# Optimization experiments

Hardware: AMD Instinct MI355X
Metric: run time of the kernel (lower is better)

## Reference

```python
import jax, jax.numpy as jnp
import numpy as np

EPS = 1e-08


def setup_inputs() -> dict:
    key = jax.random.key(0)
    ks = jax.random.split(key, 9)
    B, T, H, W = 128, 32, 32, 32
    Z = 128
    d = {}
    d['x_seq'] = jax.random.normal(ks[0], (B, T, H, W), dtype=jnp.float32)
    # encoder MLP: 1024 -> 256 -> 128 (kaiming-ish scale)
    d['We1'] = jax.random.normal(ks[1], (H * W, 256), dtype=jnp.float32) * (2.0 / (H * W)) ** 0.5
    d['be1'] = jnp.zeros((256,), jnp.float32)
    d['We2'] = jax.random.normal(ks[2], (256, Z), dtype=jnp.float32) * (2.0 / 256) ** 0.5
    d['be2'] = jnp.zeros((Z,), jnp.float32)
    # context norm params
    d['gamma'] = jnp.ones((Z,), jnp.float32)
    d['beta'] = jnp.zeros((Z,), jnp.float32)
    # g_theta: (128+1)*2=258 -> 512 -> 256
    d['Wg1'] = jax.random.normal(ks[3], (258, 512), dtype=jnp.float32) * (2.0 / 258) ** 0.5
    d['bg1'] = jnp.zeros((512,), jnp.float32)
    d['Wg2'] = jax.random.normal(ks[4], (512, 256), dtype=jnp.float32) * (2.0 / 512) ** 0.5
    d['bg2'] = jnp.zeros((256,), jnp.float32)
    # f_phi: 256 -> 256 -> y_dim=4
    d['Wf'] = jax.random.normal(ks[5], (256, 256), dtype=jnp.float32) * (2.0 / 256) ** 0.5
    d['bf'] = jnp.zeros((256,), jnp.float32)
    d['Wy'] = jax.random.normal(ks[6], (256, 4), dtype=jnp.float32) * (1.0 / 256) ** 0.5
    d['by'] = jnp.zeros((4,), jnp.float32)
    return d


def reference(x_seq, We1, be1, We2, be2, gamma, beta, Wg1, bg1, Wg2, bg2, Wf, bf, Wy, by):
    B, T, H, W = x_seq.shape
    # Encoder (MLP stand-in), vectorized over the sequence dim
    x = x_seq.reshape(B, T, H * W)
    h = jax.nn.relu(jnp.einsum('btd,dk->btk', x, We1) + be1)
    z = jnp.einsum('btk,kz->btz', h, We2) + be2          # [B,T,128]
    # Context norm over the sequence dim (torch .var() is unbiased, ddof=1)
    mu = z.mean(axis=1, keepdims=True)
    sigma = jnp.sqrt(z.var(axis=1, keepdims=True, ddof=1) + EPS)
    z = (z - mu) / sigma * gamma + beta
    # Append temporal tag
    tag = jnp.broadcast_to(jnp.arange(T, dtype=z.dtype)[None, :, None], (B, T, 1))
    z = jnp.concatenate([z, tag], axis=2)                # [B,T,129]
    # Relation network over all T^2 ordered pairs, batched as one GEMM.
    # g_hidden = relu([z_i, z_j] @ Wg1 + bg1); split Wg1 to avoid materializing the concat.
    Wg1_a, Wg1_b = Wg1[:129], Wg1[129:]
    gi = jnp.einsum('bic,ch->bih', z, Wg1_a)             # [B,T,512]
    gj = jnp.einsum('bjc,ch->bjh', z, Wg1_b)             # [B,T,512]
    g_hidden = jax.nn.relu(gi[:, :, None, :] + gj[:, None, :, :] + bg1)  # [B,T,T,512]
    g_out = jax.nn.relu(jnp.einsum('bijh,hg->bijg', g_hidden, Wg2) + bg2)
    all_g = g_out.sum(axis=(1, 2))                       # [B,256]
    f_hidden = jax.nn.relu(all_g @ Wf + bf)
    y_pred_linear = f_hidden @ Wy + by                   # [B,4]
    y_pred = jnp.argmax(y_pred_linear, axis=1)
    return (y_pred_linear, y_pred)
```

## Files before the change

### kernel.cpp

```cpp
#include <hip/hip_runtime.h>
#include <hip/hip_bf16.h>

#define EPS 1e-8f

typedef __attribute__((ext_vector_type(8))) short short8;
typedef __attribute__((ext_vector_type(4))) float f32x4;
typedef __attribute__((ext_vector_type(16))) float f32x16;

__device__ __forceinline__ unsigned short f2bf(float f) {
  union { float f; unsigned u; } v; v.f = f;
  unsigned r = v.u + 0x7fffu + ((v.u >> 16) & 1u);
  return (unsigned short)(r >> 16);
}
__device__ __forceinline__ float bf2f(unsigned short b) {
  union { unsigned u; float f; } v; v.u = ((unsigned)b) << 16;
  return v.f;
}
__device__ __forceinline__ unsigned pack_bf2(float lo, float hi) {
  unsigned r;
  asm("v_cvt_pk_bf16_f32 %0, %1, %2" : "=v"(r) : "v"(lo), "v"(hi));
  return r;
}

__global__ __launch_bounds__(256) void k0_prep(const float* __restrict__ We1,
                                               const float* __restrict__ We2,
                                               const float* __restrict__ Wg1,
                                               const float* __restrict__ Wg2,
                                               const float* __restrict__ Wf,
                                               unsigned short* __restrict__ We1T,
                                               unsigned short* __restrict__ We2T,
                                               unsigned short* __restrict__ Wg1T,
                                               unsigned short* __restrict__ Wg2T,
                                               unsigned short* __restrict__ WfT) {
  int idx = blockIdx.x * 256 + threadIdx.x;
  if (idx < 262144) {
    int n = idx >> 10, k = idx & 1023;
    We1T[idx] = f2bf(We1[k * 256 + n]);
  } else if (idx < 294912) {
    int e = idx - 262144;
    int n = e >> 8, k = e & 255;
    We2T[e] = f2bf(We2[k * 128 + n]);
  } else if (idx < 458752) {
    int e = idx - 294912;
    int n = e / 160, c = e % 160;
    float v = 0.f;
    if (c < 129) v = (n < 512) ? Wg1[c * 512 + n] : Wg1[(129 + c) * 512 + (n - 512)];
    Wg1T[e] = f2bf(v);
  } else if (idx < 589824) {
    int e = idx - 458752;
    int n = e >> 9, k = e & 511;
    Wg2T[e] = f2bf(Wg2[k * 256 + n]);
  } else {
    int e = idx - 589824;
    int n = e >> 8, k = e & 255;
    WfT[e] = f2bf(Wf[k * 256 + n]);
  }
}

__global__ __launch_bounds__(512, 2) void k1(const float* __restrict__ x,
                                             const unsigned short* __restrict__ We1T,
                                             const float* __restrict__ be1,
                                             unsigned short* __restrict__ h_bf) {
  __shared__ unsigned char As[2][8192];
  int tid = threadIdx.x, lane = tid & 63, w = tid >> 6;
  int m0 = blockIdx.x * 16;
  int srow = tid >> 5, skk = (tid & 31) * 8;
  int cb = w * 32;
  int row = lane & 15, kg = (lane >> 4) * 8;

  f32x4 acc[2] = {{0,0,0,0},{0,0,0,0}};

  auto stage = [&](int kc, int buf) {
    const float* src = x + (size_t)(m0 + srow) * 1024 + kc * 256 + skk;
    float4 a = *reinterpret_cast<const float4*>(src);
    float4 b = *reinterpret_cast<const float4*>(src + 4);
    uint4 pv;
    pv.x = pack_bf2(a.x, a.y); pv.y = pack_bf2(a.z, a.w);
    pv.z = pack_bf2(b.x, b.y); pv.w = pack_bf2(b.z, b.w);
    int addr = (srow * 512 + skk * 2) ^ ((srow & 7) << 4);
    *reinterpret_cast<uint4*>(&As[buf][addr]) = pv;
  };

  stage(0, 0);
  __syncthreads();
  for (int kc = 0; kc < 4; ++kc) {
    if (kc < 3) stage(kc + 1, (kc + 1) & 1);
    short8 breg[2][8];
#pragma unroll
    for (int cf = 0; cf < 2; ++cf)
#pragma unroll
      for (int ks = 0; ks < 8; ++ks)
        breg[cf][ks] = *reinterpret_cast<const short8*>(
            We1T + (size_t)(cb + cf * 16 + row) * 1024 + kc * 256 + ks * 32 + kg);
    const unsigned char* hc = &As[kc & 1][0];
#pragma unroll
    for (int ks = 0; ks < 8; ++ks) {
      int aoff = (row * 512 + ks * 64 + kg * 2) ^ ((row & 7) << 4);
      short8 af = *reinterpret_cast<const short8*>(hc + aoff);
      acc[0] = __builtin_amdgcn_mfma_f32_16x16x32_bf16(af, breg[0][ks], acc[0], 0, 0, 0);
      acc[1] = __builtin_amdgcn_mfma_f32_16x16x32_bf16(af, breg[1][ks], acc[1], 0, 0, 0);
    }
    __syncthreads();
  }
#pragma unroll
  for (int cf = 0; cf < 2; ++cf) {
    int col = cb + cf * 16 + row;
    float bias = be1[col];
#pragma unroll
    for (int r = 0; r < 4; ++r) {
      int orow = m0 + (lane >> 4) * 4 + r;
      h_bf[(size_t)orow * 256 + col] = f2bf(fmaxf(acc[cf][r] + bias, 0.f));
    }
  }
}

__global__ __launch_bounds__(256) void k2(const unsigned short* __restrict__ h_bf,
                                          const unsigned short* __restrict__ We2T,
                                          const float* __restrict__ be2,
                                          const float* __restrict__ gamma,
                                          const float* __restrict__ beta,
                                          const unsigned short* __restrict__ Wg1T,
                                          const float* __restrict__ bg1,
                                          unsigned short* __restrict__ g_all) {
  __shared__ unsigned char zcs[16384];
  __shared__ float zb[32][132];
  int b = blockIdx.x >> 2, nq = blockIdx.x & 3;
  int tid = threadIdx.x, lane = tid & 63, w = tid >> 6;
  int row = lane & 15, kg = (lane >> 4) * 8;

  {
    int srow = tid >> 3, skk = (tid & 7) * 32;
#pragma unroll
    for (int q = 0; q < 4; ++q) {
      short8 v = *reinterpret_cast<const short8*>(
          h_bf + (size_t)(b * 32 + srow) * 256 + skk + q * 8);
      int addr = (srow * 512 + (skk + q * 8) * 2) ^ ((srow & 7) << 4);
      *reinterpret_cast<short8*>(&zcs[addr]) = v;
    }
  }
  short8 breg1[2][8];
#pragma unroll
  for (int cf = 0; cf < 2; ++cf)
#pragma unroll
    for (int ks = 0; ks < 8; ++ks)
      breg1[cf][ks] = *reinterpret_cast<const short8*>(
          We2T + (size_t)(w * 32 + cf * 16 + row) * 256 + ks * 32 + kg);
  __syncthreads();

  {
    f32x4 acc[2][2] = {{{0,0,0,0},{0,0,0,0}},{{0,0,0,0},{0,0,0,0}}};
#pragma unroll
    for (int ks = 0; ks < 8; ++ks) {
      int a0off = (row * 512 + ks * 64 + kg * 2) ^ ((row & 7) << 4);
      int a1off = ((16 + row) * 512 + ks * 64 + kg * 2) ^ ((row & 7) << 4);
      short8 a0 = *reinterpret_cast<const short8*>(&zcs[a0off]);
      short8 a1 = *reinterpret_cast<const short8*>(&zcs[a1off]);
#pragma unroll
      for (int cf = 0; cf < 2; ++cf) {
        acc[0][cf] = __builtin_amdgcn_mfma_f32_16x16x32_bf16(a0, breg1[cf][ks], acc[0][cf], 0, 0, 0);
        acc[1][cf] = __builtin_amdgcn_mfma_f32_16x16x32_bf16(a1, breg1[cf][ks], acc[1][cf], 0, 0, 0);
      }
    }
#pragma unroll
    for (int rf = 0; rf < 2; ++rf)
#pragma unroll
      for (int cf = 0; cf < 2; ++cf) {
        int col = w * 32 + cf * 16 + row;
        float bias = be2[col];
#pragma unroll
        for (int r = 0; r < 4; ++r)
          zb[rf * 16 + (lane >> 4) * 4 + r][col] = acc[rf][cf][r] + bias;
      }
  }
  __syncthreads();

  if (tid < 128) {
    float s = 0.f, s2 = 0.f;
#pragma unroll 4
    for (int t = 0; t < 32; ++t) { float v = zb[t][tid]; s += v; s2 += v * v; }
    float mu = s * (1.f / 32.f);
    float var = (s2 - 32.f * mu * mu) * (1.f / 31.f);
    float rs = 1.f / sqrtf(fmaxf(var, 0.f) + EPS);
    float g = gamma[tid], be = beta[tid];
#pragma unroll 4
    for (int t = 0; t < 32; ++t) {
      unsigned short v = f2bf((zb[t][tid] - mu) * rs * g + be);
      int addr = (t * 512 + tid * 2) ^ ((t & 7) << 4);
      *reinterpret_cast<unsigned short*>(&zcs[addr]) = v;
    }
  } else if (tid < 160) {
    for (int t = 0; t < 32; ++t) {
      unsigned short v = (tid == 128) ? f2bf((float)t) : 0;
      int addr = (t * 512 + tid * 2) ^ ((t & 7) << 4);
      *reinterpret_cast<unsigned short*>(&zcs[addr]) = v;
    }
  }
  __syncthreads();

  {
    int n0 = nq * 256 + w * 64;
    short8 af[2][5];
#pragma unroll
    for (int rf = 0; rf < 2; ++rf)
#pragma unroll
      for (int ks = 0; ks < 5; ++ks) {
        int aoff = ((rf * 16 + row) * 512 + ks * 64 + kg * 2) ^ ((row & 7) << 4);
        af[rf][ks] = *reinterpret_cast<const short8*>(&zcs[aoff]);
      }
    short8 breg[4][5];
#pragma unroll
    for (int cf = 0; cf < 4; ++cf)
#pragma unroll
      for (int ks = 0; ks < 5; ++ks)
        breg[cf][ks] = *reinterpret_cast<const short8*>(
            Wg1T + (size_t)(n0 + cf * 16 + row) * 160 + ks * 32 + kg);
    f32x4 acc[2][4] = {{{0,0,0,0},{0,0,0,0},{0,0,0,0},{0,0,0,0}},
                       {{0,0,0,0},{0,0,0,0},{0,0,0,0},{0,0,0,0}}};
#pragma unroll
    for (int ks = 0; ks < 5; ++ks)
#pragma unroll
      for (int cf = 0; cf < 4; ++cf) {
        acc[0][cf] = __builtin_amdgcn_mfma_f32_16x16x32_bf16(af[0][ks], breg[cf][ks], acc[0][cf], 0, 0, 0);
        acc[1][cf] = __builtin_amdgcn_mfma_f32_16x16x32_bf16(af[1][ks], breg[cf][ks], acc[1][cf], 0, 0, 0);
      }
#pragma unroll
    for (int cf = 0; cf < 4; ++cf) {
      int n = n0 + cf * 16 + row;
      float bias = (n < 512) ? bg1[n] : 0.f;
#pragma unroll
      for (int rf = 0; rf < 2; ++rf)
#pragma unroll
        for (int r = 0; r < 4; ++r) {
          int t = rf * 16 + (lane >> 4) * 4 + r;
          g_all[((size_t)(b * 32 + t) << 10) + n] = f2bf(acc[rf][cf][r] + bias);
        }
    }
  }
}

__global__ __launch_bounds__(512, 2) void k3(const unsigned short* __restrict__ g_all,
                                             const unsigned short* __restrict__ Wg2T,
                                             const float* __restrict__ bg2,
                                             float* __restrict__ all_gp) {
  __shared__ unsigned char ldsH[2][32768];
  int b = blockIdx.x >> 1, hi = blockIdx.x & 1;
  int ii0 = hi * 16;
  int tid = threadIdx.x, lane = tid & 63, w = tid >> 6;
  int l31 = lane & 31, lhi = lane >> 5;
  int cb = w * 32;
  int p = tid >> 4, kslot = tid & 15;

  short8 breg[32];
#pragma unroll
  for (int s = 0; s < 32; ++s)
    breg[s] = *reinterpret_cast<const short8*>(
        Wg2T + (size_t)(cb + l31) * 512 + s * 16 + lhi * 8);

  float gjf[32];
  {
    const unsigned short* gjp = g_all + ((size_t)(b * 32 + p) << 10) + 512 + kslot * 8;
#pragma unroll
    for (int q = 0; q < 4; ++q) {
      short8 gv0 = *reinterpret_cast<const short8*>(gjp + q * 128);
#pragma unroll
      for (int e = 0; e < 8; ++e) gjf[q * 8 + e] = bf2f((unsigned short)gv0[e]);
    }
  }
  float bias = bg2[cb + l31];
  float accsum = 0.f;

  short8 gv[4];
  auto hload = [&](int ii) {
    const unsigned short* gi = g_all + ((size_t)(b * 32 + ii) << 10) + kslot * 8;
#pragma unroll
    for (int q = 0; q < 4; ++q)
      gv[q] = *reinterpret_cast<const short8*>(gi + q * 128);
  };
  auto hstore = [&](int buf) {
    unsigned char* hb = &ldsH[buf][0] + p * 1024;
#pragma unroll
    for (int q = 0; q < 4; ++q) {
      uint4 pv;
      float f0 = fmaxf(bf2f((unsigned short)gv[q][0]) + gjf[q * 8 + 0], 0.f);
      float f1 = fmaxf(bf2f((unsigned short)gv[q][1]) + gjf[q * 8 + 1], 0.f);
      float f2 = fmaxf(bf2f((unsigned short)gv[q][2]) + gjf[q * 8 + 2], 0.f);
      float f3 = fmaxf(bf2f((unsigned short)gv[q][3]) + gjf[q * 8 + 3], 0.f);
      float f4 = fmaxf(bf2f((unsigned short)gv[q][4]) + gjf[q * 8 + 4], 0.f);
      float f5 = fmaxf(bf2f((unsigned short)gv[q][5]) + gjf[q * 8 + 5], 0.f);
      float f6 = fmaxf(bf2f((unsigned short)gv[q][6]) + gjf[q * 8 + 6], 0.f);
      float f7 = fmaxf(bf2f((unsigned short)gv[q][7]) + gjf[q * 8 + 7], 0.f);
      pv.x = pack_bf2(f0, f1); pv.y = pack_bf2(f2, f3);
      pv.z = pack_bf2(f4, f5); pv.w = pack_bf2(f6, f7);
      int addr = (kslot * 16 + q * 256) ^ ((p & 7) << 4);
      *reinterpret_cast<uint4*>(hb + addr) = pv;
    }
  };

  hload(ii0);
  hstore(0);
  __syncthreads();

  for (int it = 0; it < 16; ++it) {
    if (it < 15) hload(ii0 + it + 1);
    const unsigned char* hc = &ldsH[it & 1][0];
    f32x16 acc = {0.f,0.f,0.f,0.f,0.f,0.f,0.f,0.f,0.f,0.f,0.f,0.f,0.f,0.f,0.f,0.f};
    short8 ar[4];
#pragma unroll
    for (int s = 0; s < 4; ++s)
      ar[s] = *reinterpret_cast<const short8*>(
          hc + ((l31 * 1024 + s * 32 + lhi * 16) ^ ((l31 & 7) << 4)));
#pragma unroll
    for (int s = 0; s < 32; ++s) {
      short8 cur = ar[s & 3];
      if (s < 28)
        ar[s & 3] = *reinterpret_cast<const short8*>(
            hc + ((l31 * 1024 + (s + 4) * 32 + lhi * 16) ^ ((l31 & 7) << 4)));
      __builtin_amdgcn_s_setprio(1);
      acc = __builtin_amdgcn_mfma_f32_32x32x16_bf16(cur, breg[s], acc, 0, 0, 0);
      __builtin_amdgcn_s_setprio(0);
    }
    if (it < 15) hstore((it + 1) & 1);
#pragma unroll
    for (int r = 0; r < 16; ++r)
      accsum += fmaxf(acc[r] + bias, 0.f);
    __syncthreads();
  }

  accsum += __shfl_xor(accsum, 32, 64);
  if (lane < 32)
    all_gp[(size_t)(hi * 128 + b) * 256 + cb + l31] = accsum;
}

__global__ __launch_bounds__(512) void k4(const float* __restrict__ all_gp,
                                          const unsigned short* __restrict__ WfT,
                                          const float* __restrict__ bfv,
                                          const float* __restrict__ Wy,
                                          const float* __restrict__ by,
                                          float* __restrict__ out) {
  __shared__ unsigned char As[8192];
  __shared__ float fh[16][264];
  __shared__ float wys[1024];
  __shared__ float yvs[16][4];
  int tid = threadIdx.x, lane = tid & 63, w = tid >> 6;
  int row = lane & 15, kg = (lane >> 4) * 8;
  int m0 = blockIdx.x * 16;

  {
    int r = tid >> 5, c8 = (tid & 31) * 8;
    const float* p0 = all_gp + (size_t)(m0 + r) * 256 + c8;
    const float* p1 = all_gp + (size_t)(128 + m0 + r) * 256 + c8;
    float4 a0 = *reinterpret_cast<const float4*>(p0);
    float4 a1 = *reinterpret_cast<const float4*>(p0 + 4);
    float4 b0 = *reinterpret_cast<const float4*>(p1);
    float4 b1 = *reinterpret_cast<const float4*>(p1 + 4);
    uint4 pv;
    pv.x = pack_bf2(a0.x + b0.x, a0.y + b0.y);
    pv.y = pack_bf2(a0.z + b0.z, a0.w + b0.w);
    pv.z = pack_bf2(a1.x + b1.x, a1.y + b1.y);
    pv.w = pack_bf2(a1.z + b1.z, a1.w + b1.w);
    int addr = (r * 512 + c8 * 2) ^ ((r & 7) << 4);
    *reinterpret_cast<uint4*>(&As[addr]) = pv;
  }
  wys[tid] = Wy[tid];
  wys[tid + 512] = Wy[tid + 512];
  short8 breg[2][8];
#pragma unroll
  for (int cf = 0; cf < 2; ++cf)
#pragma unroll
    for (int ks = 0; ks < 8; ++ks)
      breg[cf][ks] = *reinterpret_cast<const short8*>(
          WfT + (size_t)(w * 32 + cf * 16 + row) * 256 + ks * 32 + kg);
  __syncthreads();

  f32x4 acc[2] = {{0,0,0,0},{0,0,0,0}};
#pragma unroll
  for (int ks = 0; ks < 8; ++ks) {
    int aoff = (row * 512 + ks * 64 + kg * 2) ^ ((row & 7) << 4);
    short8 af = *reinterpret_cast<const short8*>(&As[aoff]);
    acc[0] = __builtin_amdgcn_mfma_f32_16x16x32_bf16(af, breg[0][ks], acc[0], 0, 0, 0);
    acc[1] = __builtin_amdgcn_mfma_f32_16x16x32_bf16(af, breg[1][ks], acc[1], 0, 0, 0);
  }
#pragma unroll
  for (int cf = 0; cf < 2; ++cf) {
    int col = w * 32 + cf * 16 + row;
    float bias = bfv[col];
#pragma unroll
    for (int r = 0; r < 4; ++r)
      fh[(lane >> 4) * 4 + r][col] = fmaxf(acc[cf][r] + bias, 0.f);
  }
  __syncthreads();

  if (tid < 64) {
    int r = tid >> 2, o = tid & 3;
    float y = by[o];
#pragma unroll 4
    for (int k = 0; k < 256; ++k) y += fh[r][k] * wys[k * 4 + o];
    yvs[r][o] = y;
    out[(m0 + r) * 4 + o] = y;
  }
  __syncthreads();
  if (tid < 16) {
    int am = 0;
    float best = yvs[tid][0];
#pragma unroll
    for (int o = 1; o < 4; ++o)
      if (yvs[tid][o] > best) { best = yvs[tid][o]; am = o; }
    out[512 + m0 + tid] = (float)am;
  }
}

extern "C" void kernel_launch(void* const* d_in, const int* in_sizes, int n_in,
                              void* d_out, int out_size, void* d_ws, size_t ws_size,
                              hipStream_t stream) {
  const float* x     = (const float*)d_in[0];
  const float* We1   = (const float*)d_in[1];
  const float* be1   = (const float*)d_in[2];
  const float* We2   = (const float*)d_in[3];
  const float* be2   = (const float*)d_in[4];
  const float* gamma = (const float*)d_in[5];
  const float* beta  = (const float*)d_in[6];
  const float* Wg1   = (const float*)d_in[7];
  const float* bg1   = (const float*)d_in[8];
  const float* Wg2   = (const float*)d_in[9];
  const float* bg2   = (const float*)d_in[10];
  const float* Wf    = (const float*)d_in[11];
  const float* bff   = (const float*)d_in[12];
  const float* Wy    = (const float*)d_in[13];
  const float* by    = (const float*)d_in[14];

  char* ws = (char*)d_ws;
  unsigned short* h_bf  = (unsigned short*)(ws + 0);
  unsigned short* g_all = (unsigned short*)(ws + 2097152);
  unsigned short* We1T  = (unsigned short*)(ws + 10485760);
  unsigned short* We2T  = (unsigned short*)(ws + 11010048);
  unsigned short* Wg1T  = (unsigned short*)(ws + 11075584);
  unsigned short* Wg2T  = (unsigned short*)(ws + 11403264);
  float*          all_gp= (float*)(ws + 11665408);
  unsigned short* WfT   = (unsigned short*)(ws + 11927552);
  float*          out   = (float*)d_out;

  k0_prep<<<2560, 256, 0, stream>>>(We1, We2, Wg1, Wg2, Wf, We1T, We2T, Wg1T, Wg2T, WfT);
  k1<<<256, 512, 0, stream>>>(x, We1T, be1, h_bf);
  k2<<<512, 256, 0, stream>>>(h_bf, We2T, be2, gamma, beta, Wg1T, bg1, g_all);
  k3<<<256, 512, 0, stream>>>(g_all, Wg2T, bg2, all_gp);
  k4<<<8, 512, 0, stream>>>(all_gp, WfT, bff, Wy, by, out);
}
```

Baseline: 88.62 us.

## Warp-specialize k3 with producer waves building relu tiles and 16x16 MFMA consumers

Splits the relation-network kernel into 8 MFMA consumer waves and 4 producer waves. The producer waves load gi/gj rows, apply add+relu, and write the double-buffered LDS tile, while the consumer waves switch from 32x32x16 to 16x16x32 MFMAs with a 2x2 fragment layout. The goal is to take the global loads and elementwise prep off the critical path of the matrix waves. In exchange the block grows to 768 threads with a tighter occupancy target, which adds register pressure on the consumer waves.

```diff
diff --git a/kernel.cpp b/kernel.cpp
--- a/kernel.cpp
+++ b/kernel.cpp
@@ -5,7 +5,6 @@
 
 typedef __attribute__((ext_vector_type(8))) short short8;
 typedef __attribute__((ext_vector_type(4))) float f32x4;
-typedef __attribute__((ext_vector_type(16))) float f32x16;
 
 __device__ __forceinline__ unsigned short f2bf(float f) {
   union { float f; unsigned u; } v; v.f = f;
@@ -238,97 +237,111 @@
   }
 }
 
-__global__ __launch_bounds__(512, 2) void k3(const unsigned short* __restrict__ g_all,
+__global__ __launch_bounds__(768, 3) void k3(const unsigned short* __restrict__ g_all,
                                              const unsigned short* __restrict__ Wg2T,
                                              const float* __restrict__ bg2,
                                              float* __restrict__ all_gp) {
   __shared__ unsigned char ldsH[2][32768];
   int b = blockIdx.x >> 1, hi = blockIdx.x & 1;
   int ii0 = hi * 16;
-  int tid = threadIdx.x, lane = tid & 63, w = tid >> 6;
-  int l31 = lane & 31, lhi = lane >> 5;
-  int cb = w * 32;
-  int p = tid >> 4, kslot = tid & 15;
-
-  short8 breg[32];
-#pragma unroll
-  for (int s = 0; s < 32; ++s)
-    breg[s] = *reinterpret_cast<const short8*>(
-        Wg2T + (size_t)(cb + l31) * 512 + s * 16 + lhi * 8);
-
-  float gjf[32];
-  {
-    const unsigned short* gjp = g_all + ((size_t)(b * 32 + p) << 10) + 512 + kslot * 8;
-#pragma unroll
-    for (int q = 0; q < 4; ++q) {
-      short8 gv0 = *reinterpret_cast<const short8*>(gjp + q * 128);
-#pragma unroll
-      for (int e = 0; e < 8; ++e) gjf[q * 8 + e] = bf2f((unsigned short)gv0[e]);
-    }
-  }
-  float bias = bg2[cb + l31];
-  float accsum = 0.f;
-
-  short8 gv[4];
-  auto hload = [&](int ii) {
-    const unsigned short* gi = g_all + ((size_t)(b * 32 + ii) << 10) + kslot * 8;
-#pragma unroll
-    for (int q = 0; q < 4; ++q)
-      gv[q] = *reinterpret_cast<const short8*>(gi + q * 128);
-  };
-  auto hstore = [&](int buf) {
-    unsigned char* hb = &ldsH[buf][0] + p * 1024;
-#pragma unroll
-    for (int q = 0; q < 4; ++q) {
-      uint4 pv;
-      float f0 = fmaxf(bf2f((unsigned short)gv[q][0]) + gjf[q * 8 + 0], 0.f);
-      float f1 = fmaxf(bf2f((unsigned short)gv[q][1]) + gjf[q * 8 + 1], 0.f);
-      float f2 = fmaxf(bf2f((unsigned short)gv[q][2]) + gjf[q * 8 + 2], 0.f);
-      float f3 = fmaxf(bf2f((unsigned short)gv[q][3]) + gjf[q * 8 + 3], 0.f);
-      float f4 = fmaxf(bf2f((unsigned short)gv[q][4]) + gjf[q * 8 + 4], 0.f);
-      float f5 = fmaxf(bf2f((unsigned short)gv[q][5]) + gjf[q * 8 + 5], 0.f);
-      float f6 = fmaxf(bf2f((unsigned short)gv[q][6]) + gjf[q * 8 + 6], 0.f);
-      float f7 = fmaxf(bf2f((unsigned short)gv[q][7]) + gjf[q * 8 + 7], 0.f);
-      pv.x = pack_bf2(f0, f1); pv.y = pack_bf2(f2, f3);
-      pv.z = pack_bf2(f4, f5); pv.w = pack_bf2(f6, f7);
-      int addr = (kslot * 16 + q * 256) ^ ((p & 7) << 4);
-      *reinterpret_cast<uint4*>(hb + addr) = pv;
-    }
-  };
-
-  hload(ii0);
-  hstore(0);
-  __syncthreads();
-
-  for (int it = 0; it < 16; ++it) {
-    if (it < 15) hload(ii0 + it + 1);
-    const unsigned char* hc = &ldsH[it & 1][0];
-    f32x16 acc = {0.f,0.f,0.f,0.f,0.f,0.f,0.f,0.f,0.f,0.f,0.f,0.f,0.f,0.f,0.f,0.f};
-    short8 ar[4];
-#pragma unroll
-    for (int s = 0; s < 4; ++s)
-      ar[s] = *reinterpret_cast<const short8*>(
-          hc + ((l31 * 1024 + s * 32 + lhi * 16) ^ ((l31 & 7) << 4)));
-#pragma unroll
-    for (int s = 0; s < 32; ++s) {
-      short8 cur = ar[s & 3];
-      if (s < 28)
-        ar[s & 3] = *reinterpret_cast<const short8*>(
-            hc + ((l31 * 1024 + (s + 4) * 32 + lhi * 16) ^ ((l31 & 7) << 4)));
-      __builtin_amdgcn_s_setprio(1);
-      acc = __builtin_amdgcn_mfma_f32_32x32x16_bf16(cur, breg[s], acc, 0, 0, 0);
-      __builtin_amdgcn_s_setprio(0);
-    }
-    if (it < 15) hstore((it + 1) & 1);
-#pragma unroll
-    for (int r = 0; r < 16; ++r)
-      accsum += fmaxf(acc[r] + bias, 0.f);
+  int tid = threadIdx.x;
+
+  if (tid < 512) {
+    int lane = tid & 63, w = tid >> 6;
+    int row = lane & 15, kg = (lane >> 4) * 8;
+    int cb = w * 32;
+    short8 breg[2][16];
+#pragma unroll
+    for (int cf = 0; cf < 2; ++cf)
+#pragma unroll
+      for (int ks = 0; ks < 16; ++ks)
+        breg[cf][ks] = *reinterpret_cast<const short8*>(
+            Wg2T + (size_t)(cb + cf * 16 + row) * 512 + ks * 32 + kg);
+    float biasv[2] = { bg2[cb + row], bg2[cb + 16 + row] };
+    float accsum[2] = { 0.f, 0.f };
     __syncthreads();
-  }
-
-  accsum += __shfl_xor(accsum, 32, 64);
-  if (lane < 32)
-    all_gp[(size_t)(hi * 128 + b) * 256 + cb + l31] = accsum;
+
+    for (int it = 0; it < 16; ++it) {
+      const unsigned char* hc = &ldsH[it & 1][0];
+      f32x4 acc[2][2] = {{{0,0,0,0},{0,0,0,0}},{{0,0,0,0},{0,0,0,0}}};
+      short8 a0 = *reinterpret_cast<const short8*>(hc + ((row * 1024 + kg * 2) ^ ((row & 7) << 4)));
+      short8 a1 = *reinterpret_cast<const short8*>(hc + (((16 + row) * 1024 + kg * 2) ^ ((row & 7) << 4)));
+#pragma unroll
+      for (int ks = 0; ks < 16; ++ks) {
+        short8 c0v = a0, c1v = a1;
+        if (ks < 15) {
+          a0 = *reinterpret_cast<const short8*>(hc + ((row * 1024 + (ks + 1) * 64 + kg * 2) ^ ((row & 7) << 4)));
+          a1 = *reinterpret_cast<const short8*>(hc + (((16 + row) * 1024 + (ks + 1) * 64 + kg * 2) ^ ((row & 7) << 4)));
+        }
+        __builtin_amdgcn_s_setprio(1);
+        acc[0][0] = __builtin_amdgcn_mfma_f32_16x16x32_bf16(c0v, breg[0][ks], acc[0][0], 0, 0, 0);
+        acc[0][1] = __builtin_amdgcn_mfma_f32_16x16x32_bf16(c0v, breg[1][ks], acc[0][1], 0, 0, 0);
+        acc[1][0] = __builtin_amdgcn_mfma_f32_16x16x32_bf16(c1v, breg[0][ks], acc[1][0], 0, 0, 0);
+        acc[1][1] = __builtin_amdgcn_mfma_f32_16x16x32_bf16(c1v, breg[1][ks], acc[1][1], 0, 0, 0);
+        __builtin_amdgcn_s_setprio(0);
+      }
+#pragma unroll
+      for (int cf = 0; cf < 2; ++cf)
+#pragma unroll
+        for (int rf = 0; rf < 2; ++rf)
+#pragma unroll
+          for (int r = 0; r < 4; ++r)
+            accsum[cf] += fmaxf(acc[rf][cf][r] + biasv[cf], 0.f);
+      __syncthreads();
+    }
+
+    accsum[0] += __shfl_xor(accsum[0], 16, 64);
+    accsum[0] += __shfl_xor(accsum[0], 32, 64);
+    accsum[1] += __shfl_xor(accsum[1], 16, 64);
+    accsum[1] += __shfl_xor(accsum[1], 32, 64);
+    if ((lane >> 4) == 0) {
+      all_gp[(size_t)(hi * 128 + b) * 256 + cb + lane] = accsum[0];
+      all_gp[(size_t)(hi * 128 + b) * 256 + cb + 16 + lane] = accsum[1];
+    }
+  } else {
+    int ptid = tid - 512;
+    int prow = ptid >> 3;
+    int pk = ptid & 7;
+    const unsigned short* gjp = g_all + ((size_t)(b * 32 + prow) << 10) + 512 + pk * 8;
+    short8 gjr[8];
+#pragma unroll
+    for (int c = 0; c < 8; ++c)
+      gjr[c] = *reinterpret_cast<const short8*>(gjp + c * 64);
+    unsigned char* hb0 = &ldsH[0][0] + prow * 1024;
+    unsigned char* hb1 = &ldsH[1][0] + prow * 1024;
+    const unsigned short* gbase = g_all + ((size_t)(b * 32) << 10) + pk * 8;
+
+    auto fill = [&](unsigned char* hb, int ii) {
+      const unsigned short* gi = gbase + ((size_t)ii << 10);
+      short8 gv[8];
+#pragma unroll
+      for (int c = 0; c < 8; ++c)
+        gv[c] = *reinterpret_cast<const short8*>(gi + c * 64);
+#pragma unroll
+      for (int c = 0; c < 8; ++c) {
+        float f0 = fmaxf(bf2f((unsigned short)gv[c][0]) + bf2f((unsigned short)gjr[c][0]), 0.f);
+        float f1 = fmaxf(bf2f((unsigned short)gv[c][1]) + bf2f((unsigned short)gjr[c][1]), 0.f);
+        float f2 = fmaxf(bf2f((unsigned short)gv[c][2]) + bf2f((unsigned short)gjr[c][2]), 0.f);
+        float f3 = fmaxf(bf2f((unsigned short)gv[c][3]) + bf2f((unsigned short)gjr[c][3]), 0.f);
+        float f4 = fmaxf(bf2f((unsigned short)gv[c][4]) + bf2f((unsigned short)gjr[c][4]), 0.f);
+        float f5 = fmaxf(bf2f((unsigned short)gv[c][5]) + bf2f((unsigned short)gjr[c][5]), 0.f);
+        float f6 = fmaxf(bf2f((unsigned short)gv[c][6]) + bf2f((unsigned short)gjr[c][6]), 0.f);
+        float f7 = fmaxf(bf2f((unsigned short)gv[c][7]) + bf2f((unsigned short)gjr[c][7]), 0.f);
+        uint4 pv;
+        pv.x = pack_bf2(f0, f1); pv.y = pack_bf2(f2, f3);
+        pv.z = pack_bf2(f4, f5); pv.w = pack_bf2(f6, f7);
+        int addr = (pk * 16 + c * 128) ^ ((prow & 7) << 4);
+        *reinterpret_cast<uint4*>(hb + addr) = pv;
+      }
+    };
+
+    fill(hb0, ii0);
+    __syncthreads();
+    for (int it = 0; it < 16; ++it) {
+      if (it < 15) fill((it & 1) ? hb0 : hb1, ii0 + it + 1);
+      __syncthreads();
+    }
+  }
 }
 
 __global__ __launch_bounds__(512) void k4(const float* __restrict__ all_gp,
@@ -442,6 +455,6 @@
   k0_prep<<<2560, 256, 0, stream>>>(We1, We2, Wg1, Wg2, Wf, We1T, We2T, Wg1T, Wg2T, WfT);
   k1<<<256, 512, 0, stream>>>(x, We1T, be1, h_bf);
   k2<<<512, 256, 0, stream>>>(h_bf, We2T, be2, gamma, beta, Wg1T, bg1, g_all);
-  k3<<<256, 512, 0, stream>>>(g_all, Wg2T, bg2, all_gp);
+  k3<<<256, 768, 0, stream>>>(g_all, Wg2T, bg2, all_gp);
   k4<<<8, 512, 0, stream>>>(all_gp, WfT, bff, Wy, by, out);
 }
```

Measured after the change: 102.2 us. 15.3% more time.

## Split relation GEMM into quarter blocks and switch to 16x16x32 MFMA tiles

Applied to the files above, without the earlier changes.

The relation-network kernel now uses four blocks per batch item, each covering 8 i-rows instead of 16, which doubles the grid to 512 blocks to fill more compute units. The inner GEMM changes from one 32x32x16 MFMA per k-step to four 16x16x32 MFMAs over a 2x2 fragment tile, with the B fragments and accumulator layout reorganised to match. The final reduction sums four partial outputs instead of two, and the workspace offset for the Wf transpose moves to make room. The cost is that the Wg2 register preload and the gj setup are repeated in twice as many blocks.

```diff
diff --git a/kernel.cpp b/kernel.cpp
--- a/kernel.cpp
+++ b/kernel.cpp
@@ -5,7 +5,6 @@
 
 typedef __attribute__((ext_vector_type(8))) short short8;
 typedef __attribute__((ext_vector_type(4))) float f32x4;
-typedef __attribute__((ext_vector_type(16))) float f32x16;
 
 __device__ __forceinline__ unsigned short f2bf(float f) {
   union { float f; unsigned u; } v; v.f = f;
@@ -243,18 +242,20 @@
                                              const float* __restrict__ bg2,
                                              float* __restrict__ all_gp) {
   __shared__ unsigned char ldsH[2][32768];
-  int b = blockIdx.x >> 1, hi = blockIdx.x & 1;
-  int ii0 = hi * 16;
+  int b = blockIdx.x >> 2, qi = blockIdx.x & 3;
+  int ii0 = qi * 8;
   int tid = threadIdx.x, lane = tid & 63, w = tid >> 6;
-  int l31 = lane & 31, lhi = lane >> 5;
+  int row = lane & 15, kg = (lane >> 4) * 8;
   int cb = w * 32;
   int p = tid >> 4, kslot = tid & 15;
 
-  short8 breg[32];
-#pragma unroll
-  for (int s = 0; s < 32; ++s)
-    breg[s] = *reinterpret_cast<const short8*>(
-        Wg2T + (size_t)(cb + l31) * 512 + s * 16 + lhi * 8);
+  short8 breg[2][16];
+#pragma unroll
+  for (int cf = 0; cf < 2; ++cf)
+#pragma unroll
+    for (int ks = 0; ks < 16; ++ks)
+      breg[cf][ks] = *reinterpret_cast<const short8*>(
+          Wg2T + (size_t)(cb + cf * 16 + row) * 512 + ks * 32 + kg);
 
   float gjf[32];
   {
@@ -266,8 +267,8 @@
       for (int e = 0; e < 8; ++e) gjf[q * 8 + e] = bf2f((unsigned short)gv0[e]);
     }
   }
-  float bias = bg2[cb + l31];
-  float accsum = 0.f;
+  float biasv[2] = { bg2[cb + row], bg2[cb + 16 + row] };
+  float accsum[2] = { 0.f, 0.f };
 
   short8 gv[4];
   auto hload = [&](int ii) {
@@ -300,35 +301,47 @@
   hstore(0);
   __syncthreads();
 
-  for (int it = 0; it < 16; ++it) {
-    if (it < 15) hload(ii0 + it + 1);
+  for (int it = 0; it < 8; ++it) {
+    if (it < 7) hload(ii0 + it + 1);
     const unsigned char* hc = &ldsH[it & 1][0];
-    f32x16 acc = {0.f,0.f,0.f,0.f,0.f,0.f,0.f,0.f,0.f,0.f,0.f,0.f,0.f,0.f,0.f,0.f};
-    short8 ar[4];
-#pragma unroll
-    for (int s = 0; s < 4; ++s)
-      ar[s] = *reinterpret_cast<const short8*>(
-          hc + ((l31 * 1024 + s * 32 + lhi * 16) ^ ((l31 & 7) << 4)));
-#pragma unroll
-    for (int s = 0; s < 32; ++s) {
-      short8 cur = ar[s & 3];
-      if (s < 28)
-        ar[s & 3] = *reinterpret_cast<const short8*>(
-            hc + ((l31 * 1024 + (s + 4) * 32 + lhi * 16) ^ ((l31 & 7) << 4)));
+    f32x4 acc[2][2] = {{{0,0,0,0},{0,0,0,0}},{{0,0,0,0},{0,0,0,0}}};
+    short8 a0 = *reinterpret_cast<const short8*>(hc + ((row * 1024 + kg * 2) ^ ((row & 7) << 4)));
+    short8 a1 = *reinterpret_cast<const short8*>(hc + (((16 + row) * 1024 + kg * 2) ^ ((row & 7) << 4)));
+#pragma unroll
+    for (int ks = 0; ks < 16; ++ks) {
+      short8 c0v = a0, c1v = a1;
+      if (ks < 15) {
+        a0 = *reinterpret_cast<const short8*>(hc + ((row * 1024 + (ks + 1) * 64 + kg * 2) ^ ((row & 7) << 4)));
+        a1 = *reinterpret_cast<const short8*>(hc + (((16 + row) * 1024 + (ks + 1) * 64 + kg * 2) ^ ((row & 7) << 4)));
+      }
       __builtin_amdgcn_s_setprio(1);
-      acc = __builtin_amdgcn_mfma_f32_32x32x16_bf16(cur, breg[s], acc, 0, 0, 0);
+      acc[0][0] = __builtin_amdgcn_mfma_f32_16x16x32_bf16(c0v, breg[0][ks], acc[0][0], 0, 0, 0);
+      acc[0][1] = __builtin_amdgcn_mfma_f32_16x16x32_bf16(c0v, breg[1][ks], acc[0][1], 0, 0, 0);
+      acc[1][0] = __builtin_amdgcn_mfma_f32_16x16x32_bf16(c1v, breg[0][ks], acc[1][0], 0, 0, 0);
+      acc[1][1] = __builtin_amdgcn_mfma_f32_16x16x32_bf16(c1v, breg[1][ks], acc[1][1], 0, 0, 0);
       __builtin_amdgcn_s_setprio(0);
     }
-    if (it < 15) hstore((it + 1) & 1);
-#pragma unroll
-    for (int r = 0; r < 16; ++r)
-      accsum += fmaxf(acc[r] + bias, 0.f);
+    if (it < 7) hstore((it + 1) & 1);
+#pragma unroll
+    for (int cf = 0; cf < 2; ++cf)
+#pragma unroll
+      for (int rf = 0; rf < 2; ++rf)
+#pragma unroll
+        for (int r = 0; r < 4; ++r)
+          accsum[cf] += fmaxf(acc[rf][cf][r] + biasv[cf], 0.f);
     __syncthreads();
   }
 
-  accsum += __shfl_xor(accsum, 32, 64);
-  if (lane < 32)
-    all_gp[(size_t)(hi * 128 + b) * 256 + cb + l31] = accsum;
+#pragma unroll
+  for (int cf = 0; cf < 2; ++cf) {
+    accsum[cf] += __shfl_xor(accsum[cf], 16, 64);
+    accsum[cf] += __shfl_xor(accsum[cf], 32, 64);
+  }
+  if ((lane >> 4) == 0) {
+#pragma unroll
+    for (int cf = 0; cf < 2; ++cf)
+      all_gp[(size_t)(qi * 128 + b) * 256 + cb + cf * 16 + lane] = accsum[cf];
+  }
 }
 
 __global__ __launch_bounds__(512) void k4(const float* __restrict__ all_gp,
@@ -347,17 +360,20 @@
 
   {
     int r = tid >> 5, c8 = (tid & 31) * 8;
-    const float* p0 = all_gp + (size_t)(m0 + r) * 256 + c8;
-    const float* p1 = all_gp + (size_t)(128 + m0 + r) * 256 + c8;
-    float4 a0 = *reinterpret_cast<const float4*>(p0);
-    float4 a1 = *reinterpret_cast<const float4*>(p0 + 4);
-    float4 b0 = *reinterpret_cast<const float4*>(p1);
-    float4 b1 = *reinterpret_cast<const float4*>(p1 + 4);
+    float s[8];
+#pragma unroll
+    for (int e = 0; e < 8; ++e) s[e] = 0.f;
+#pragma unroll
+    for (int q = 0; q < 4; ++q) {
+      const float* p0 = all_gp + (size_t)(q * 128 + m0 + r) * 256 + c8;
+      float4 a0 = *reinterpret_cast<const float4*>(p0);
+      float4 a1 = *reinterpret_cast<const float4*>(p0 + 4);
+      s[0] += a0.x; s[1] += a0.y; s[2] += a0.z; s[3] += a0.w;
+      s[4] += a1.x; s[5] += a1.y; s[6] += a1.z; s[7] += a1.w;
+    }
     uint4 pv;
-    pv.x = pack_bf2(a0.x + b0.x, a0.y + b0.y);
-    pv.y = pack_bf2(a0.z + b0.z, a0.w + b0.w);
-    pv.z = pack_bf2(a1.x + b1.x, a1.y + b1.y);
-    pv.w = pack_bf2(a1.z + b1.z, a1.w + b1.w);
+    pv.x = pack_bf2(s[0], s[1]); pv.y = pack_bf2(s[2], s[3]);
+    pv.z = pack_bf2(s[4], s[5]); pv.w = pack_bf2(s[6], s[7]);
     int addr = (r * 512 + c8 * 2) ^ ((r & 7) << 4);
     *reinterpret_cast<uint4*>(&As[addr]) = pv;
   }
@@ -436,12 +452,12 @@
   unsigned short* Wg1T  = (unsigned short*)(ws + 11075584);
   unsigned short* Wg2T  = (unsigned short*)(ws + 11403264);
   float*          all_gp= (float*)(ws + 11665408);
-  unsigned short* WfT   = (unsigned short*)(ws + 11927552);
+  unsigned short* WfT   = (unsigned short*)(ws + 12189696);
   float*          out   = (float*)d_out;
 
   k0_prep<<<2560, 256, 0, stream>>>(We1, We2, Wg1, Wg2, Wf, We1T, We2T, Wg1T, Wg2T, WfT);
   k1<<<256, 512, 0, stream>>>(x, We1T, be1, h_bf);
   k2<<<512, 256, 0, stream>>>(h_bf, We2T, be2, gamma, beta, Wg1T, bg1, g_all);
-  k3<<<256, 512, 0, stream>>>(g_all, Wg2T, bg2, all_gp);
+  k3<<<512, 512, 0, stream>>>(g_all, Wg2T, bg2, all_gp);
   k4<<<8, 512, 0, stream>>>(all_gp, WfT, bff, Wy, by, out);
 }
```

Result: slower. 92.38 us (+4.2%).
